# Kernel tuning notes

Measured on AMD Instinct MI355X. Metric: run time of the kernel, lower is better.

## Reference

```python
import jax, jax.numpy as jnp
import numpy as np

PC_RANGE = (-50.0, -50.0, -4.0, 50.0, 50.0, 4.0)
IMG_H, IMG_W = 256.0, 704.0
EPS = 1e-5


def _bilinear_sample(feat, u, v):
    # feat [H,W,C]; u,v [M] in [0,1]; matches F.grid_sample(align_corners=False, padding_mode='zeros')
    H, W, _ = feat.shape
    x = u * W - 0.5
    y = v * H - 0.5
    x0 = jnp.floor(x)
    y0 = jnp.floor(y)
    dx = (x - x0)[:, None]
    dy = (y - y0)[:, None]
    x0 = x0.astype(jnp.int32)
    y0 = y0.astype(jnp.int32)

    def g(xi, yi):
        inb = ((xi >= 0) & (xi < W) & (yi >= 0) & (yi < H)).astype(feat.dtype)[:, None]
        return feat[jnp.clip(yi, 0, H - 1), jnp.clip(xi, 0, W - 1)] * inb

    return (g(x0, y0) * (1 - dx) * (1 - dy) + g(x0 + 1, y0) * dx * (1 - dy)
            + g(x0, y0 + 1) * (1 - dx) * dy + g(x0 + 1, y0 + 1) * dx * dy)


def _conv1x1(t, w, b):
    return jnp.einsum('bchw,oc->bohw', t, w) + b[None, :, None, None]


def _inorm(t, eps=1e-5):
    # InstanceNorm2d (affine=False): normalize per (b, c) over spatial dims
    m = t.mean(axis=(2, 3), keepdims=True)
    var = t.var(axis=(2, 3), keepdims=True)
    return (t - m) * jax.lax.rsqrt(var + eps)


def _forward(feat, lidar2img, bev_pos, pe_w1, pe_b1, pe_w2, pe_b2, pe_w3, pe_b3,
             c1_w, c1_b, c2_w, c2_b, c3_w, c3_b):
    B, N, C, Hf, Wf = feat.shape
    _, P, Hb, Wb, _ = bev_pos.shape
    Q = Hb * Wb
    lo = jnp.asarray(PC_RANGE[:3], feat.dtype)
    hi = jnp.asarray(PC_RANGE[3:], feat.dtype)
    # 'b p h w d -> b (h w) p d', then scale normalized coords into pc_range
    ref01 = jnp.transpose(bev_pos, (0, 2, 3, 1, 4)).reshape(B, Q, P, 3)
    ref = ref01 * (hi - lo) + lo
    # project through per-camera lidar2img (homogeneous)
    pts = jnp.concatenate([ref, jnp.ones_like(ref[..., :1])], axis=-1)  # [B,Q,P,4]
    cam = jnp.einsum('bnij,bqpj->bnqpi', lidar2img, pts)                # [B,N,Q,P,4]
    homo = cam[..., 2]
    z = jnp.maximum(homo, EPS)
    u = cam[..., 0] / z / IMG_W
    v = cam[..., 1] / z / IMG_H
    valid = ((homo > EPS) & (u > 0.0) & (u < 1.0) & (v > 0.0) & (v < 1.0)).astype(feat.dtype)
    # bilinear gather per camera; feats to channel-last ('b n (g c) h w -> (b g) n h w c', G=1)
    fmap = jnp.transpose(feat, (0, 1, 3, 4, 2)).reshape(B * N, Hf, Wf, C)
    samp = jax.vmap(_bilinear_sample)(fmap, u.reshape(B * N, Q * P), v.reshape(B * N, Q * P))
    samp = samp.reshape(B, N, Q, P, C) * valid[..., None]
    samp = samp.sum(axis=1)  # sum over cameras -> [B,Q,P,C]
    # PositionalEncodingMap(3 -> 256 -> 256 -> 128) on normalized reference points
    pe = jax.nn.relu(ref01 @ pe_w1 + pe_b1)
    pe = jax.nn.relu(pe @ pe_w2 + pe_b2)
    pe = pe @ pe_w3 + pe_b3
    samp = samp + pe
    # 'b (h w) g p c -> b (p g c) h w' with g=1
    x = jnp.transpose(samp.reshape(B, Hb, Wb, P, C), (0, 3, 4, 1, 2)).reshape(B, P * C, Hb, Wb)
    gelu = lambda t: jax.nn.gelu(t, approximate=False)
    x = gelu(_inorm(_conv1x1(x, c1_w, c1_b)))
    x = gelu(_inorm(_conv1x1(x, c2_w, c2_b)))
    x = _conv1x1(x, c3_w, c3_b)
    return x


def setup_inputs() -> dict:
    key = jax.random.key(0)
    ks = jax.random.split(key, 16)
    B, N, C, Hf, Wf = 1, 6, 128, 32, 88
    P, Hb, Wb = 4, 160, 160
    E = 128
    MID = 256
    s = 0.02
    return {
        'feat': jax.random.normal(ks[0], (B, N, C, Hf, Wf), jnp.float32),
        'lidar2img': jax.random.normal(ks[1], (B, N, 4, 4), jnp.float32),
        'bev_pos': jax.random.uniform(ks[2], (B, P, Hb, Wb, 3), jnp.float32),
        'pe_w1': jax.random.normal(ks[3], (3, MID), jnp.float32) * s,
        'pe_b1': jnp.zeros((MID,), jnp.float32),
        'pe_w2': jax.random.normal(ks[4], (MID, MID), jnp.float32) * s,
        'pe_b2': jnp.zeros((MID,), jnp.float32),
        'pe_w3': jax.random.normal(ks[5], (MID, E), jnp.float32) * s,
        'pe_b3': jnp.zeros((E,), jnp.float32),
        'c1_w': jax.random.normal(ks[6], (4 * E, P * 128), jnp.float32) * s,
        'c1_b': jnp.zeros((4 * E,), jnp.float32),
        'c2_w': jax.random.normal(ks[7], (E, 4 * E), jnp.float32) * s,
        'c2_b': jnp.zeros((E,), jnp.float32),
        'c3_w': jax.random.normal(ks[8], (E, E), jnp.float32) * s,
        'c3_b': jnp.zeros((E,), jnp.float32),
    }


def reference(feat, lidar2img, bev_pos, pe_w1, pe_b1, pe_w2, pe_b2, pe_w3, pe_b3,
              c1_w, c1_b, c2_w, c2_b, c3_w, c3_b):
    return _forward(feat, lidar2img, bev_pos, pe_w1, pe_b1, pe_w2, pe_b2, pe_w3, pe_b3,
                    c1_w, c1_b, c2_w, c2_b, c3_w, c3_b)
```

## Files before the change

kernel.cpp:

```cpp
#include <hip/hip_runtime.h>
#include <cstdint>
#include <cstddef>

using frag8 = __attribute__((ext_vector_type(8))) short;
using f32x4 = __attribute__((ext_vector_type(4))) float;

__device__ __forceinline__ float b2f_bits(unsigned short u) {
    union { uint32_t u32; float f; } x; x.u32 = ((uint32_t)u) << 16; return x.f;
}
__device__ __forceinline__ float b2f_lo(uint32_t pk) {
    return __builtin_bit_cast(float, pk << 16);
}
__device__ __forceinline__ float b2f_hi(uint32_t pk) {
    return __builtin_bit_cast(float, pk & 0xffff0000u);
}
__device__ __forceinline__ unsigned short f2b(float f) {
    uint32_t u = __builtin_bit_cast(uint32_t, f);
    uint32_t r = (u + 0x7fffu + ((u >> 16) & 1u)) >> 16;
    return (unsigned short)r;
}

#define HF 32
#define WFEAT 88
#define NCAM 6
#define NPT 102400
#define BM 128
#define BN 128
#define BK 64

__global__ __launch_bounds__(256) void k_prep(const float* __restrict__ feat,
                                              const float* __restrict__ pw2,
                                              const float* __restrict__ pw3,
                                              const float* __restrict__ c1w,
                                              const float* __restrict__ c2w,
                                              const float* __restrict__ c3w,
                                              const float* __restrict__ pw1,
                                              const float* __restrict__ pb1,
                                              const float* __restrict__ l2i,
                                              const float* __restrict__ bev,
                                              unsigned short* __restrict__ featT,
                                              unsigned short* __restrict__ W2Tb,
                                              unsigned short* __restrict__ W3Tb,
                                              unsigned short* __restrict__ C1Wb,
                                              unsigned short* __restrict__ C2Wb,
                                              unsigned short* __restrict__ C3Wb,
                                              float* __restrict__ w1p,
                                              int* __restrict__ poff,
                                              float4* __restrict__ pwts) {
    int b = blockIdx.x, t = threadIdx.x;
    if (b < 2400) {
        int idx = b * 256 + t;
        int n = idx / NPT, pt = idx - n * NPT;
        int q = pt >> 2, p = pt & 3;
        int h = q / 160, w = q - h * 160;
        const float* bv = bev + ((p * 160 + h) * 160 + w) * 3;
        float rx = bv[0] * 100.f - 50.f;
        float ry = bv[1] * 100.f - 50.f;
        float rz = bv[2] * 8.f - 4.f;
        const float* M = l2i + n * 16;
        float c0   = M[0] * rx + M[1] * ry + M[2]  * rz + M[3];
        float c1v  = M[4] * rx + M[5] * ry + M[6]  * rz + M[7];
        float homo = M[8] * rx + M[9] * ry + M[10] * rz + M[11];
        float z = fmaxf(homo, 1e-5f);
        float u = c0 / z / 704.0f;
        float v = c1v / z / 256.0f;
        if (!(homo > 1e-5f && u > 0.f && u < 1.f && v > 0.f && v < 1.f)) {
            poff[idx] = -1;
            return;
        }
        float fx = u * (float)WFEAT - 0.5f;
        float fy = v * (float)HF - 0.5f;
        float fx0 = floorf(fx), fy0 = floorf(fy);
        float dx = fx - fx0, dy = fy - fy0;
        int x0 = (int)fx0, y0 = (int)fy0;
        float wxa = (x0 < 0) ? dx : 1.f - dx;
        float wxb = (x0 >= 0 && x0 < WFEAT - 1) ? dx : 0.f;
        float wya = (y0 < 0) ? dy : 1.f - dy;
        float wyb = (y0 >= 0 && y0 < HF - 1) ? dy : 0.f;
        int bx = max(x0, 0), by = max(y0, 0);
        poff[idx] = ((n * HF + by) * WFEAT + bx) << 7;
        pwts[idx] = make_float4(wxa * wya, wxb * wya, wxa * wyb, wxb * wyb);
        return;
    }
    b -= 2400;
    if (b < 8448) {
        int idx = b * 256 + t;
        int c = idx & 127;
        int rest = idx >> 7;
        int x = rest % WFEAT; rest /= WFEAT;
        int y = rest % HF;
        int n = rest / HF;
        featT[idx] = f2b(feat[((n * 128 + c) * HF + y) * WFEAT + x]);
        return;
    }
    b -= 8448;
    if (b < 256) {
        int idx = b * 256 + t;
        int r = idx >> 8, c = idx & 255;
        W2Tb[c * 256 + r] = f2b(pw2[idx]);
        return;
    }
    b -= 256;
    if (b < 128) {
        int idx = b * 256 + t;
        int r = idx >> 7, c = idx & 127;
        W3Tb[c * 256 + r] = f2b(pw3[idx]);
        return;
    }
    b -= 128;
    if (b < 1024) { int idx = b * 256 + t; C1Wb[idx] = f2b(c1w[idx]); return; }
    b -= 1024;
    if (b < 256)  { int idx = b * 256 + t; C2Wb[idx] = f2b(c2w[idx]); return; }
    b -= 256;
    if (b < 64)   { int idx = b * 256 + t; C3Wb[idx] = f2b(c3w[idx]); return; }
    w1p[t * 4 + 0] = pw1[t];
    w1p[t * 4 + 1] = pw1[256 + t];
    w1p[t * 4 + 2] = pw1[512 + t];
    w1p[t * 4 + 3] = pb1[t];
}

__global__ __launch_bounds__(256) void k_sample2(const unsigned short* __restrict__ featT,
                                                 const int* __restrict__ poff,
                                                 const float4* __restrict__ pwts,
                                                 unsigned short* __restrict__ samp) {
    int pt = blockIdx.x * 4 + (threadIdx.x >> 6);
    int lane = threadIdx.x & 63;
    int c2 = lane * 2;
    int offs[NCAM];
    float4 ww[NCAM];
    #pragma unroll
    for (int n = 0; n < NCAM; ++n) offs[n] = poff[n * NPT + pt];
    #pragma unroll
    for (int n = 0; n < NCAM; ++n) ww[n] = pwts[n * NPT + pt];
    float acc0 = 0.f, acc1 = 0.f;
    #pragma unroll
    for (int n = 0; n < NCAM; ++n) {
        if (offs[n] >= 0) {
            const unsigned short* base = featT + offs[n] + c2;
            uint32_t p00 = *(const uint32_t*)(base);
            uint32_t p01 = *(const uint32_t*)(base + 128);
            uint32_t p10 = *(const uint32_t*)(base + WFEAT * 128);
            uint32_t p11 = *(const uint32_t*)(base + WFEAT * 128 + 128);
            float4 w = ww[n];
            acc0 += w.x * b2f_lo(p00) + w.y * b2f_lo(p01) + w.z * b2f_lo(p10) + w.w * b2f_lo(p11);
            acc1 += w.x * b2f_hi(p00) + w.y * b2f_hi(p01) + w.z * b2f_hi(p10) + w.w * b2f_hi(p11);
        }
    }
    uint32_t outpk = (uint32_t)f2b(acc0) | ((uint32_t)f2b(acc1) << 16);
    *(uint32_t*)(samp + (size_t)pt * 128 + c2) = outpk;
}

__device__ __forceinline__ void stage_tile_big(const unsigned short* __restrict__ g, int ld,
                                               unsigned short* lds, int t) {
    int r = t >> 2, cs = t & 3;
    int cl = cs ^ ((r >> 1) & 3);
    __builtin_amdgcn_global_load_lds(
        (const __attribute__((address_space(1))) void*)(g + (size_t)r * ld + cl * 8),
        (__attribute__((address_space(3))) void*)(lds + (t >> 6) * 512),
        16, 0, 0);
}

__device__ __forceinline__ frag8 frag_read_big(const unsigned short* lds, int row, int chunk) {
    return *(const frag8*)(lds + row * 32 + ((chunk ^ ((row >> 1) & 3)) << 3));
}

__device__ __forceinline__ void mma_tile_big(const unsigned short* As, const unsigned short* Bs,
                                             int wm, int wn, int lane, f32x4 (&acc)[4][4]) {
    int lm = lane & 15, lq = lane >> 4;
    frag8 a[4], b[4];
    #pragma unroll
    for (int t = 0; t < 4; ++t) a[t] = frag_read_big(As, wm * 64 + t * 16 + lm, lq);
    #pragma unroll
    for (int t = 0; t < 4; ++t) b[t] = frag_read_big(Bs, wn * 64 + t * 16 + lm, lq);
    #pragma unroll
    for (int tm = 0; tm < 4; ++tm)
        #pragma unroll
        for (int tn = 0; tn < 4; ++tn)
            acc[tm][tn] = __builtin_amdgcn_mfma_f32_16x16x32_bf16(a[tm], b[tn], acc[tm][tn], 0, 0, 0);
}

__global__ __launch_bounds__(1024) void k_gemm_pe2f(const float* __restrict__ bev,
                                                    const float* __restrict__ w1p,
                                                    const unsigned short* __restrict__ Bt,
                                                    const float* __restrict__ bias,
                                                    unsigned short* __restrict__ H2) {
    __shared__ unsigned short As[2][256 * 32], Bs[2][256 * 32];
    int t = threadIdx.x, lane = t & 63, wid = t >> 6;
    int wm = wid >> 2, wn = wid & 3;
    int m0 = blockIdx.x * 256;
    int r = t >> 2, cs = t & 3;
    int cl = cs ^ ((r >> 1) & 3);
    int m = m0 + r;
    int q = m >> 2, p = m & 3;
    int h = q / 160, w = q - h * 160;
    const float* bv = bev + ((p * 160 + h) * 160 + w) * 3;
    float cx = bv[0], cy = bv[1], cz = bv[2];

    f32x4 acc[4][4] = {};
    {
        int o = cl * 8;
        union { unsigned short u[8]; frag8 v; } pk;
        #pragma unroll
        for (int j = 0; j < 8; ++j) {
            float4 wv = *(const float4*)(w1p + (o + j) * 4);
            float a = fmaf(cx, wv.x, fmaf(cy, wv.y, fmaf(cz, wv.z, wv.w)));
            pk.u[j] = f2b(fmaxf(a, 0.f));
        }
        *(frag8*)(&As[0][r * 32 + cs * 8]) = pk.v;
    }
    stage_tile_big(Bt, 256, Bs[0], t);
    __syncthreads();
    #pragma unroll
    for (int kt = 0; kt < 8; ++kt) {
        int cur = kt & 1, nxt = cur ^ 1;
        if (kt + 1 < 8) {
            int o = (kt + 1) * 32 + cl * 8;
            union { unsigned short u[8]; frag8 v; } pk;
            #pragma unroll
            for (int j = 0; j < 8; ++j) {
                float4 wv = *(const float4*)(w1p + (o + j) * 4);
                float a = fmaf(cx, wv.x, fmaf(cy, wv.y, fmaf(cz, wv.z, wv.w)));
                pk.u[j] = f2b(fmaxf(a, 0.f));
            }
            *(frag8*)(&As[nxt][r * 32 + cs * 8]) = pk.v;
            stage_tile_big(Bt + (kt + 1) * 32, 256, Bs[nxt], t);
        }
        mma_tile_big(As[cur], Bs[cur], wm, wn, lane, acc);
        __syncthreads();
    }
    int lm = lane & 15, lq = lane >> 4;
    #pragma unroll
    for (int tn = 0; tn < 4; ++tn) {
        int n = wn * 64 + tn * 16 + lm;
        float bn = bias[n];
        #pragma unroll
        for (int tm = 0; tm < 4; ++tm) {
            int mb = m0 + wm * 64 + tm * 16 + lq * 4;
            #pragma unroll
            for (int rr = 0; rr < 4; ++rr)
                H2[(size_t)(mb + rr) * 256 + n] = f2b(fmaxf(acc[tm][tn][rr] + bn, 0.f));
        }
    }
}

template <int KT>
__device__ __forceinline__ void gemm_loop_big(const unsigned short* __restrict__ A, int ldA,
                                              const unsigned short* __restrict__ B, int ldB,
                                              unsigned short (*As)[256 * 32],
                                              unsigned short (*Bs)[256 * 32],
                                              int t, int wm, int wn, int lane,
                                              f32x4 (&acc)[4][4]) {
    stage_tile_big(A, ldA, As[0], t);
    stage_tile_big(B, ldB, Bs[0], t);
    __syncthreads();
    #pragma unroll
    for (int kt = 0; kt < KT; ++kt) {
        int cur = kt & 1, nxt = cur ^ 1;
        if (kt + 1 < KT) {
            stage_tile_big(A + (kt + 1) * 32, ldA, As[nxt], t);
            stage_tile_big(B + (kt + 1) * 32, ldB, Bs[nxt], t);
        }
        mma_tile_big(As[cur], Bs[cur], wm, wn, lane, acc);
        __syncthreads();
    }
}

__global__ __launch_bounds__(1024) void k_gemm_conv1_big(const unsigned short* __restrict__ A,
                                                         const unsigned short* __restrict__ Bt,
                                                         const float* __restrict__ bias,
                                                         unsigned short* __restrict__ Y,
                                                         float* __restrict__ st) {
    __shared__ unsigned short As[2][256 * 32], Bs[2][256 * 32];
    int t = threadIdx.x, lane = t & 63, wid = t >> 6;
    int wm = wid >> 2, wn = wid & 3;
    int m0 = blockIdx.x * 256, n0 = blockIdx.y * 256;
    f32x4 acc[4][4] = {};
    gemm_loop_big<16>(A + (size_t)m0 * 512, 512, Bt + (size_t)n0 * 512, 512,
                      As, Bs, t, wm, wn, lane, acc);
    int lm = lane & 15, lq = lane >> 4;
    #pragma unroll
    for (int tn = 0; tn < 4; ++tn) {
        int n = n0 + wn * 64 + tn * 16 + lm;
        float bn = bias[n];
        float s1 = 0.f, s2 = 0.f;
        #pragma unroll
        for (int tm = 0; tm < 4; ++tm) {
            int mb = m0 + wm * 64 + tm * 16 + lq * 4;
            #pragma unroll
            for (int rr = 0; rr < 4; ++rr) {
                float v = acc[tm][tn][rr] + bn;
                Y[(size_t)(mb + rr) * 512 + n] = f2b(v);
                s1 += v; s2 += v * v;
            }
        }
        s1 += __shfl_xor(s1, 16); s1 += __shfl_xor(s1, 32);
        s2 += __shfl_xor(s2, 16); s2 += __shfl_xor(s2, 32);
        if (lq == 0) { atomicAdd(&st[n], s1); atomicAdd(&st[512 + n], s2); }
    }
}

__device__ __forceinline__ void stage_tile(const unsigned short* __restrict__ g, int ld,
                                           unsigned short* lds, int wave, int lane) {
    #pragma unroll
    for (int j = 0; j < 4; ++j) {
        int idx = wave * 256 + j * 64 + lane;
        int r = idx >> 3;
        int cs = idx & 7;
        int cl = cs ^ (r & 7);
        __builtin_amdgcn_global_load_lds(
            (const __attribute__((address_space(1))) void*)(g + (size_t)r * ld + cl * 8),
            (__attribute__((address_space(3))) void*)(lds + wave * 2048 + j * 512),
            16, 0, 0);
    }
}

__device__ __forceinline__ frag8 frag_read(const unsigned short* lds, int row, int chunk) {
    return *(const frag8*)(lds + row * 64 + ((chunk ^ (row & 7)) << 3));
}

__device__ __forceinline__ void mma_tile(const unsigned short* As, const unsigned short* Bs,
                                         int wm, int wn, int lane, f32x4 (&acc)[4][4]) {
    int lm = lane & 15, lq = lane >> 4;
    #pragma unroll
    for (int kk = 0; kk < 2; ++kk) {
        frag8 a[4], b[4];
        #pragma unroll
        for (int t = 0; t < 4; ++t) a[t] = frag_read(As, wm * 64 + t * 16 + lm, kk * 4 + lq);
        #pragma unroll
        for (int t = 0; t < 4; ++t) b[t] = frag_read(Bs, wn * 64 + t * 16 + lm, kk * 4 + lq);
        #pragma unroll
        for (int tm = 0; tm < 4; ++tm)
            #pragma unroll
            for (int tn = 0; tn < 4; ++tn)
                acc[tm][tn] = __builtin_amdgcn_mfma_f32_16x16x32_bf16(a[tm], b[tn], acc[tm][tn], 0, 0, 0);
    }
}

__global__ __launch_bounds__(256) void k_gemm_pe3(const unsigned short* __restrict__ A,
                                                  const unsigned short* __restrict__ Bt,
                                                  const float* __restrict__ bias,
                                                  const unsigned short* __restrict__ samp,
                                                  unsigned short* __restrict__ X) {
    __shared__ unsigned short As[BM * BK], Bs[BN * BK];
    int lane = threadIdx.x & 63, wave = threadIdx.x >> 6;
    int wm = wave >> 1, wn = wave & 1;
    int m0 = blockIdx.x * BM;
    f32x4 acc[4][4] = {};
    for (int kt = 0; kt < 4; ++kt) {
        stage_tile(A + (size_t)m0 * 256 + kt * BK, 256, As, wave, lane);
        stage_tile(Bt + (size_t)kt * BK, 256, Bs, wave, lane);
        __syncthreads();
        mma_tile(As, Bs, wm, wn, lane, acc);
        __syncthreads();
    }
    int lm = lane & 15, lq = lane >> 4;
    #pragma unroll
    for (int tn = 0; tn < 4; ++tn) {
        int n = wn * 64 + tn * 16 + lm;
        float bn = bias[n];
        #pragma unroll
        for (int tm = 0; tm < 4; ++tm) {
            int mb = m0 + wm * 64 + tm * 16 + lq * 4;
            #pragma unroll
            for (int rr = 0; rr < 4; ++rr) {
                size_t off = (size_t)(mb + rr) * 128 + n;
                X[off] = f2b(acc[tm][tn][rr] + bn + b2f_bits(samp[off]));
            }
        }
    }
}

template <int K, bool STATS>
__global__ __launch_bounds__(256) void k_gemm_conv(const unsigned short* __restrict__ A,
                                                   const unsigned short* __restrict__ Bt,
                                                   const float* __restrict__ bias,
                                                   unsigned short* __restrict__ Y, int ldY,
                                                   float* __restrict__ st, int C) {
    __shared__ unsigned short As[BM * BK], Bs[BN * BK];
    int lane = threadIdx.x & 63, wave = threadIdx.x >> 6;
    int wm = wave >> 1, wn = wave & 1;
    int m0 = blockIdx.x * BM, n0 = blockIdx.y * BN;
    f32x4 acc[4][4] = {};
    for (int kt = 0; kt < K / BK; ++kt) {
        stage_tile(A + (size_t)m0 * K + kt * BK, K, As, wave, lane);
        stage_tile(Bt + (size_t)n0 * K + kt * BK, K, Bs, wave, lane);
        __syncthreads();
        mma_tile(As, Bs, wm, wn, lane, acc);
        __syncthreads();
    }
    int lm = lane & 15, lq = lane >> 4;
    #pragma unroll
    for (int tn = 0; tn < 4; ++tn) {
        int n = n0 + wn * 64 + tn * 16 + lm;
        float bn = bias[n];
        float s1 = 0.f, s2 = 0.f;
        #pragma unroll
        for (int tm = 0; tm < 4; ++tm) {
            int mb = m0 + wm * 64 + tm * 16 + lq * 4;
            #pragma unroll
            for (int rr = 0; rr < 4; ++rr) {
                float v = acc[tm][tn][rr] + bn;
                Y[(size_t)(mb + rr) * ldY + n] = f2b(v);
                if (STATS) { s1 += v; s2 += v * v; }
            }
        }
        if (STATS) {
            s1 += __shfl_xor(s1, 16); s1 += __shfl_xor(s1, 32);
            s2 += __shfl_xor(s2, 16); s2 += __shfl_xor(s2, 32);
            if (lq == 0) { atomicAdd(&st[n], s1); atomicAdd(&st[C + n], s2); }
        }
    }
}

__global__ __launch_bounds__(256) void k_gemm_conv3(const unsigned short* __restrict__ A,
                                                    const unsigned short* __restrict__ Bt,
                                                    const float* __restrict__ bias,
                                                    float* __restrict__ out) {
    __shared__ unsigned short As[BM * BK], Bs[BN * BK];
    int lane = threadIdx.x & 63, wave = threadIdx.x >> 6;
    int wm = wave >> 1, wn = wave & 1;
    int m0 = blockIdx.x * BM;
    f32x4 acc[4][4] = {};
    for (int kt = 0; kt < 2; ++kt) {
        stage_tile(A + (size_t)m0 * 128 + kt * BK, 128, As, wave, lane);
        stage_tile(Bt + (size_t)kt * BK, 128, Bs, wave, lane);
        __syncthreads();
        mma_tile(As, Bs, wm, wn, lane, acc);
        __syncthreads();
    }
    int lm = lane & 15, lq = lane >> 4;
    #pragma unroll
    for (int tn = 0; tn < 4; ++tn) {
        int n = wn * 64 + tn * 16 + lm;
        float bn = bias[n];
        #pragma unroll
        for (int tm = 0; tm < 4; ++tm) {
            int mb = m0 + wm * 64 + tm * 16 + lq * 4;
            float4 pk;
            pk.x = acc[tm][tn][0] + bn;
            pk.y = acc[tm][tn][1] + bn;
            pk.z = acc[tm][tn][2] + bn;
            pk.w = acc[tm][tn][3] + bn;
            *(float4*)(out + (size_t)n * 25600 + mb) = pk;
        }
    }
}

__global__ void k_normgelu8f(const unsigned short* __restrict__ Y, const float* __restrict__ st,
                             unsigned short* __restrict__ X2, int Cmask, int C, float inv_n,
                             int total8) {
    int i8 = blockIdx.x * 256 + threadIdx.x;
    if (i8 >= total8) return;
    int e0 = i8 * 8;
    int c = e0 & Cmask;
    uint4 y = *(const uint4*)(Y + e0);
    float4 s1a = *(const float4*)(st + c);
    float4 s1b = *(const float4*)(st + c + 4);
    float4 s2a = *(const float4*)(st + C + c);
    float4 s2b = *(const float4*)(st + C + c + 4);
    float mu[8] = { s1a.x * inv_n, s1a.y * inv_n, s1a.z * inv_n, s1a.w * inv_n,
                    s1b.x * inv_n, s1b.y * inv_n, s1b.z * inv_n, s1b.w * inv_n };
    float sq[8] = { s2a.x, s2a.y, s2a.z, s2a.w, s2b.x, s2b.y, s2b.z, s2b.w };
    float rs[8];
    #pragma unroll
    for (int j = 0; j < 8; ++j) rs[j] = rsqrtf(sq[j] * inv_n - mu[j] * mu[j] + 1e-5f);
    const float is2 = 0.70710678118654752f;
    unsigned int yw[4] = {y.x, y.y, y.z, y.w};
    unsigned int ow[4];
    #pragma unroll
    for (int j = 0; j < 4; ++j) {
        float v0 = (b2f_bits((unsigned short)(yw[j] & 0xffffu)) - mu[j * 2]) * rs[j * 2];
        float v1 = (b2f_bits((unsigned short)(yw[j] >> 16)) - mu[j * 2 + 1]) * rs[j * 2 + 1];
        float g0 = 0.5f * v0 * (1.f + erff(v0 * is2));
        float g1 = 0.5f * v1 * (1.f + erff(v1 * is2));
        ow[j] = (uint32_t)f2b(g0) | ((uint32_t)f2b(g1) << 16);
    }
    *(uint4*)(X2 + e0) = make_uint4(ow[0], ow[1], ow[2], ow[3]);
}

extern "C" void kernel_launch(void* const* d_in, const int* in_sizes, int n_in,
                              void* d_out, int out_size, void* d_ws, size_t ws_size,
                              hipStream_t stream) {
    (void)in_sizes; (void)n_in; (void)out_size; (void)ws_size;
    const float* feat = (const float*)d_in[0];
    const float* l2i  = (const float*)d_in[1];
    const float* bev  = (const float*)d_in[2];
    const float* pw1  = (const float*)d_in[3];
    const float* pb1  = (const float*)d_in[4];
    const float* pw2  = (const float*)d_in[5];
    const float* pb2  = (const float*)d_in[6];
    const float* pw3  = (const float*)d_in[7];
    const float* pb3  = (const float*)d_in[8];
    const float* c1w  = (const float*)d_in[9];
    const float* c1b  = (const float*)d_in[10];
    const float* c2w  = (const float*)d_in[11];
    const float* c2b  = (const float*)d_in[12];
    const float* c3w  = (const float*)d_in[13];
    const float* c3b  = (const float*)d_in[14];
    float* outp = (float*)d_out;
    char* ws = (char*)d_ws;

    unsigned short* featT = (unsigned short*)(ws + 0);
    unsigned short* W2Tb  = (unsigned short*)(ws + 4348416);
    unsigned short* W3Tb  = (unsigned short*)(ws + 4479488);
    unsigned short* C1Wb  = (unsigned short*)(ws + 4545024);
    unsigned short* C2Wb  = (unsigned short*)(ws + 5069312);
    unsigned short* C3Wb  = (unsigned short*)(ws + 5200384);
    float* stats          = (float*)(ws + 5233152);
    float* w1p            = (float*)(ws + 5243392);
    int*    poff          = (int*)(ws + 5247488);
    float4* pwts          = (float4*)(ws + 7705088);
    char* BUF1 = ws + 17535488;
    char* BUF2 = ws + 69964288;
    char* BUF3 = ws + 122393088;

    float* st512 = stats;
    float* st128 = stats + 2048;

    unsigned short* H2   = (unsigned short*)BUF2;
    unsigned short* samp = (unsigned short*)BUF3;
    unsigned short* X    = (unsigned short*)BUF1;
    unsigned short* Y1   = (unsigned short*)BUF2;
    unsigned short* X2   = (unsigned short*)BUF3;
    unsigned short* Y2   = (unsigned short*)BUF1;
    unsigned short* X3   = (unsigned short*)(BUF1 + 6553600);

    hipMemsetAsync(stats, 0, 10240, stream);
    k_prep<<<12577, 256, 0, stream>>>(feat, pw2, pw3, c1w, c2w, c3w, pw1, pb1, l2i, bev,
                                      featT, W2Tb, W3Tb, C1Wb, C2Wb, C3Wb, w1p, poff, pwts);

    k_sample2<<<25600, 256, 0, stream>>>(featT, poff, pwts, samp);

    k_gemm_pe2f<<<400, 1024, 0, stream>>>(bev, w1p, W2Tb, pb2, H2);
    k_gemm_pe3<<<dim3(800, 1), 256, 0, stream>>>(H2, W3Tb, pb3, samp, X);

    k_gemm_conv1_big<<<dim3(100, 2), 1024, 0, stream>>>(X, C1Wb, c1b, Y1, st512);
    k_normgelu8f<<<6400, 256, 0, stream>>>(Y1, st512, X2, 511, 512, 1.f / 25600.f, 1638400);

    k_gemm_conv<512, true><<<dim3(200, 1), 256, 0, stream>>>(X2, C2Wb, c2b, Y2, 128, st128, 128);
    k_normgelu8f<<<1600, 256, 0, stream>>>(Y2, st128, X3, 127, 128, 1.f / 25600.f, 409600);

    k_gemm_conv3<<<dim3(200, 1), 256, 0, stream>>>(X3, C3Wb, c3b, outp);
}
```

Baseline: 324.6 us.

## Precompute PE layer-1 activations in prep kernel and fold stats memset

The first positional-encoding layer (3->256 linear plus ReLU) moves out of the pe2 GEMM's tile-staging loop into extra blocks of the prep kernel. Those blocks write a bf16 H1 buffer that a plain tiled GEMM then reads. The stats zeroing memset is also folded into the prep kernel's tail block, removing one launch. This trades in-register recomputation for a 51 MB write and reread of H1 through global memory, while simplifying the GEMM's staging.

```diff
diff --git a/kernel.cpp b/kernel.cpp
--- a/kernel.cpp
+++ b/kernel.cpp
@@ -44,10 +44,32 @@
                                               unsigned short* __restrict__ C1Wb,
                                               unsigned short* __restrict__ C2Wb,
                                               unsigned short* __restrict__ C3Wb,
-                                              float* __restrict__ w1p,
+                                              unsigned short* __restrict__ H1,
+                                              float* __restrict__ stats,
                                               int* __restrict__ poff,
                                               float4* __restrict__ pwts) {
     int b = blockIdx.x, t = threadIdx.x;
+    if (b < 25600) {
+        int idx = b * 256 + t;
+        int m = idx >> 6;
+        int o4 = (idx & 63) * 4;
+        int q = m >> 2, p = m & 3;
+        int h = q / 160, w = q - h * 160;
+        const float* bv = bev + ((p * 160 + h) * 160 + w) * 3;
+        float cx = bv[0], cy = bv[1], cz = bv[2];
+        float4 a0 = *(const float4*)(pw1 + o4);
+        float4 a1 = *(const float4*)(pw1 + 256 + o4);
+        float4 a2 = *(const float4*)(pw1 + 512 + o4);
+        float4 bb = *(const float4*)(pb1 + o4);
+        ushort4 o;
+        o.x = f2b(fmaxf(cx * a0.x + cy * a1.x + cz * a2.x + bb.x, 0.f));
+        o.y = f2b(fmaxf(cx * a0.y + cy * a1.y + cz * a2.y + bb.y, 0.f));
+        o.z = f2b(fmaxf(cx * a0.z + cy * a1.z + cz * a2.z + bb.z, 0.f));
+        o.w = f2b(fmaxf(cx * a0.w + cy * a1.w + cz * a2.w + bb.w, 0.f));
+        *(ushort4*)(H1 + (size_t)m * 256 + o4) = o;
+        return;
+    }
+    b -= 25600;
     if (b < 2400) {
         int idx = b * 256 + t;
         int n = idx / NPT, pt = idx - n * NPT;
@@ -113,10 +135,8 @@
     if (b < 256)  { int idx = b * 256 + t; C2Wb[idx] = f2b(c2w[idx]); return; }
     b -= 256;
     if (b < 64)   { int idx = b * 256 + t; C3Wb[idx] = f2b(c3w[idx]); return; }
-    w1p[t * 4 + 0] = pw1[t];
-    w1p[t * 4 + 1] = pw1[256 + t];
-    w1p[t * 4 + 2] = pw1[512 + t];
-    w1p[t * 4 + 3] = pb1[t];
+    #pragma unroll
+    for (int j = 0; j < 10; ++j) stats[t * 10 + j] = 0.f;
 }
 
 __global__ __launch_bounds__(256) void k_sample2(const unsigned short* __restrict__ featT,
@@ -179,70 +199,6 @@
             acc[tm][tn] = __builtin_amdgcn_mfma_f32_16x16x32_bf16(a[tm], b[tn], acc[tm][tn], 0, 0, 0);
 }
 
-__global__ __launch_bounds__(1024) void k_gemm_pe2f(const float* __restrict__ bev,
-                                                    const float* __restrict__ w1p,
-                                                    const unsigned short* __restrict__ Bt,
-                                                    const float* __restrict__ bias,
-                                                    unsigned short* __restrict__ H2) {
-    __shared__ unsigned short As[2][256 * 32], Bs[2][256 * 32];
-    int t = threadIdx.x, lane = t & 63, wid = t >> 6;
-    int wm = wid >> 2, wn = wid & 3;
-    int m0 = blockIdx.x * 256;
-    int r = t >> 2, cs = t & 3;
-    int cl = cs ^ ((r >> 1) & 3);
-    int m = m0 + r;
-    int q = m >> 2, p = m & 3;
-    int h = q / 160, w = q - h * 160;
-    const float* bv = bev + ((p * 160 + h) * 160 + w) * 3;
-    float cx = bv[0], cy = bv[1], cz = bv[2];
-
-    f32x4 acc[4][4] = {};
-    {
-        int o = cl * 8;
-        union { unsigned short u[8]; frag8 v; } pk;
-        #pragma unroll
-        for (int j = 0; j < 8; ++j) {
-            float4 wv = *(const float4*)(w1p + (o + j) * 4);
-            float a = fmaf(cx, wv.x, fmaf(cy, wv.y, fmaf(cz, wv.z, wv.w)));
-            pk.u[j] = f2b(fmaxf(a, 0.f));
-        }
-        *(frag8*)(&As[0][r * 32 + cs * 8]) = pk.v;
-    }
-    stage_tile_big(Bt, 256, Bs[0], t);
-    __syncthreads();
-    #pragma unroll
-    for (int kt = 0; kt < 8; ++kt) {
-        int cur = kt & 1, nxt = cur ^ 1;
-        if (kt + 1 < 8) {
-            int o = (kt + 1) * 32 + cl * 8;
-            union { unsigned short u[8]; frag8 v; } pk;
-            #pragma unroll
-            for (int j = 0; j < 8; ++j) {
-                float4 wv = *(const float4*)(w1p + (o + j) * 4);
-                float a = fmaf(cx, wv.x, fmaf(cy, wv.y, fmaf(cz, wv.z, wv.w)));
-                pk.u[j] = f2b(fmaxf(a, 0.f));
-            }
-            *(frag8*)(&As[nxt][r * 32 + cs * 8]) = pk.v;
-            stage_tile_big(Bt + (kt + 1) * 32, 256, Bs[nxt], t);
-        }
-        mma_tile_big(As[cur], Bs[cur], wm, wn, lane, acc);
-        __syncthreads();
-    }
-    int lm = lane & 15, lq = lane >> 4;
-    #pragma unroll
-    for (int tn = 0; tn < 4; ++tn) {
-        int n = wn * 64 + tn * 16 + lm;
-        float bn = bias[n];
-        #pragma unroll
-        for (int tm = 0; tm < 4; ++tm) {
-            int mb = m0 + wm * 64 + tm * 16 + lq * 4;
-            #pragma unroll
-            for (int rr = 0; rr < 4; ++rr)
-                H2[(size_t)(mb + rr) * 256 + n] = f2b(fmaxf(acc[tm][tn][rr] + bn, 0.f));
-        }
-    }
-}
-
 template <int KT>
 __device__ __forceinline__ void gemm_loop_big(const unsigned short* __restrict__ A, int ldA,
                                               const unsigned short* __restrict__ B, int ldB,
@@ -262,6 +218,31 @@
         }
         mma_tile_big(As[cur], Bs[cur], wm, wn, lane, acc);
         __syncthreads();
+    }
+}
+
+__global__ __launch_bounds__(1024) void k_gemm_pe2_big(const unsigned short* __restrict__ A,
+                                                       const unsigned short* __restrict__ Bt,
+                                                       const float* __restrict__ bias,
+                                                       unsigned short* __restrict__ H2) {
+    __shared__ unsigned short As[2][256 * 32], Bs[2][256 * 32];
+    int t = threadIdx.x, lane = t & 63, wid = t >> 6;
+    int wm = wid >> 2, wn = wid & 3;
+    int m0 = blockIdx.x * 256;
+    f32x4 acc[4][4] = {};
+    gemm_loop_big<8>(A + (size_t)m0 * 256, 256, Bt, 256, As, Bs, t, wm, wn, lane, acc);
+    int lm = lane & 15, lq = lane >> 4;
+    #pragma unroll
+    for (int tn = 0; tn < 4; ++tn) {
+        int n = wn * 64 + tn * 16 + lm;
+        float bn = bias[n];
+        #pragma unroll
+        for (int tm = 0; tm < 4; ++tm) {
+            int mb = m0 + wm * 64 + tm * 16 + lq * 4;
+            #pragma unroll
+            for (int rr = 0; rr < 4; ++rr)
+                H2[(size_t)(mb + rr) * 256 + n] = f2b(fmaxf(acc[tm][tn][rr] + bn, 0.f));
+        }
     }
 }
 
@@ -507,7 +488,6 @@
     unsigned short* C2Wb  = (unsigned short*)(ws + 5069312);
     unsigned short* C3Wb  = (unsigned short*)(ws + 5200384);
     float* stats          = (float*)(ws + 5233152);
-    float* w1p            = (float*)(ws + 5243392);
     int*    poff          = (int*)(ws + 5247488);
     float4* pwts          = (float4*)(ws + 7705088);
     char* BUF1 = ws + 17535488;
@@ -517,6 +497,7 @@
     float* st512 = stats;
     float* st128 = stats + 2048;
 
+    unsigned short* H1   = (unsigned short*)BUF1;
     unsigned short* H2   = (unsigned short*)BUF2;
     unsigned short* samp = (unsigned short*)BUF3;
     unsigned short* X    = (unsigned short*)BUF1;
@@ -525,13 +506,13 @@
     unsigned short* Y2   = (unsigned short*)BUF1;
     unsigned short* X3   = (unsigned short*)(BUF1 + 6553600);
 
-    hipMemsetAsync(stats, 0, 10240, stream);
-    k_prep<<<12577, 256, 0, stream>>>(feat, pw2, pw3, c1w, c2w, c3w, pw1, pb1, l2i, bev,
-                                      featT, W2Tb, W3Tb, C1Wb, C2Wb, C3Wb, w1p, poff, pwts);
+    k_prep<<<38177, 256, 0, stream>>>(feat, pw2, pw3, c1w, c2w, c3w, pw1, pb1, l2i, bev,
+                                      featT, W2Tb, W3Tb, C1Wb, C2Wb, C3Wb, H1, stats,
+                                      poff, pwts);
 
     k_sample2<<<25600, 256, 0, stream>>>(featT, poff, pwts, samp);
 
-    k_gemm_pe2f<<<400, 1024, 0, stream>>>(bev, w1p, W2Tb, pb2, H2);
+    k_gemm_pe2_big<<<400, 1024, 0, stream>>>(H1, W2Tb, pb2, H2);
     k_gemm_pe3<<<dim3(800, 1), 256, 0, stream>>>(H2, W3Tb, pb3, samp, X);
 
     k_gemm_conv1_big<<<dim3(100, 2), 1024, 0, stream>>>(X, C1Wb, c1b, Y1, st512);
```

New measurement: 287.6 us. 1.13x faster.
